# Kernel optimization log

Measured on AMD Instinct MI355X. Metric: run time of the kernel, lower is better.

The kernel has to match this reference:

```python
import jax, jax.numpy as jnp
import numpy as np

N_NODES = 100000
N_EDGES = 3200000
N_GRAPHS = 64
IN_DIM = 8
HIDDEN = 128
N_CLASSES = 10


def _glorot(key, fan_in, fan_out):
    s = 1.0 / np.sqrt(fan_in)
    return jax.random.uniform(key, (fan_in, fan_out), jnp.float32, -s, s)


def setup_inputs() -> dict:
    key = jax.random.key(0)
    ks = jax.random.split(key, 16)
    x = jax.random.normal(ks[0], (N_NODES, IN_DIM), jnp.float32)
    edge_index = jax.random.randint(ks[1], (2, N_EDGES), 0, N_NODES, jnp.int64)
    batch = jnp.sort(jax.random.randint(ks[2], (N_NODES,), 0, N_GRAPHS, jnp.int64))
    inp = {"x": x, "edge_index": edge_index, "batch": batch}
    dims = [(IN_DIM, HIDDEN)] + [(HIDDEN, HIDDEN)] * 4
    for i, (fi, fo) in enumerate(dims, start=1):
        inp[f"W{i}"] = _glorot(ks[2 + i], fi, fo)
        inp[f"b{i}"] = jnp.zeros((fo,), jnp.float32)
    inp["Wout"] = _glorot(ks[10], HIDDEN, N_CLASSES)
    inp["bout"] = jnp.zeros((N_CLASSES,), jnp.float32)
    return inp


def reference(x, edge_index, batch, W1, b1, W2, b2, W3, b3, W4, b4, W5, b5, Wout, bout):
    src, dst = edge_index[0], edge_index[1]
    E = src.shape[0]
    # GCN symmetric normalization with self-loops: deg computed on dst (col)
    deg = jax.ops.segment_sum(jnp.ones((E,), x.dtype), dst, num_segments=N_NODES) + 1.0
    dis = jax.lax.rsqrt(deg)                      # deg^{-1/2}, [N]
    enorm = dis[src] * dis[dst]                   # per-edge coeff, [E]
    self_coef = 1.0 / deg                         # self-loop coeff, [N]

    def gcn_conv(h, W, b):
        h = h @ W                                 # [N, F_out]
        msg = h[src] * enorm[:, None]             # gather + scale, [E, F_out]
        agg = jax.ops.segment_sum(msg, dst, num_segments=N_NODES)
        agg = agg + self_coef[:, None] * h        # fused self-loop term
        return agg + b

    h = jax.nn.relu(gcn_conv(x, W1, b1))
    h = jax.nn.relu(gcn_conv(h, W2, b2))
    h = jax.nn.relu(gcn_conv(h, W3, b3))
    h = jax.nn.relu(gcn_conv(h, W4, b4))
    h = jax.nn.relu(gcn_conv(h, W5, b5))

    # global mean pool per graph
    counts = jax.ops.segment_sum(jnp.ones((N_NODES,), h.dtype), batch, num_segments=N_GRAPHS)
    sums = jax.ops.segment_sum(h, batch, num_segments=N_GRAPHS)
    pooled = sums / jnp.maximum(counts, 1.0)[:, None]   # [G, HIDDEN]

    logits = pooled @ Wout + bout
    return jax.nn.log_softmax(logits, axis=1)
```

## Files before the change

kernel.cpp:

```cpp
#include <hip/hip_runtime.h>
#include <hip/hip_fp16.h>

#define N_NODES 100000
#define N_EDGES 3200000
#define N_GRAPHS 64
#define HID 128
#define NBUCK 782
#define NPART 256
#define EPB (N_EDGES / NPART)

typedef _Float16 half8 __attribute__((ext_vector_type(8)));
typedef float floatx4 __attribute__((ext_vector_type(4)));
typedef float floatx2 __attribute__((ext_vector_type(2)));

__device__ inline unsigned char f32_to_fp8(float v) {
    int p = __builtin_amdgcn_cvt_pk_fp8_f32(v, v, 0, false);
    return (unsigned char)(p & 0xff);
}

__global__ __launch_bounds__(256) void hist_kernel(const int* __restrict__ dst,
                                                   int* __restrict__ hist_g) {
    __shared__ int lh[NBUCK];
    int t = threadIdx.x, b = blockIdx.x;
    for (int j = t; j < NBUCK; j += 256) lh[j] = 0;
    __syncthreads();
    int beg = b * EPB, end = beg + EPB;
    for (int i = beg + t; i < end; i += 256) atomicAdd(&lh[dst[i] >> 7], 1);
    __syncthreads();
    for (int j = t; j < NBUCK; j += 256) hist_g[j * NPART + b] = lh[j];
}

__global__ __launch_bounds__(1024) void scan_hist(int* __restrict__ hist_g,
                                                  int* __restrict__ bb,
                                                  int* __restrict__ row_ptrN) {
    __shared__ int tot[1024];
    int t = threadIdx.x;
    int sum = 0;
    if (t < NBUCK) {
        const int4* h4 = (const int4*)(hist_g + t * NPART);
        for (int b = 0; b < NPART / 4; b++) {
            int4 v = h4[b];
            sum += v.x + v.y + v.z + v.w;
        }
    }
    tot[t] = sum;
    __syncthreads();
    for (int off = 1; off < 1024; off <<= 1) {
        int x = (t >= off) ? tot[t - off] : 0;
        __syncthreads();
        tot[t] += x;
        __syncthreads();
    }
    int excl = tot[t] - sum;
    if (t < NBUCK) {
        bb[t] = excl;
        int run = excl;
        int4* h4 = (int4*)(hist_g + t * NPART);
        for (int b = 0; b < NPART / 4; b++) {
            int4 v = h4[b];
            int4 o;
            o.x = run; run += v.x;
            o.y = run; run += v.y;
            o.z = run; run += v.z;
            o.w = run; run += v.w;
            h4[b] = o;
        }
    }
    if (t == NBUCK - 1) {
        bb[NBUCK] = excl + sum;
        row_ptrN[0] = excl + sum;
    }
}

__global__ __launch_bounds__(256) void part_kernel(const int* __restrict__ src,
                                                   const int* __restrict__ dst,
                                                   const int* __restrict__ hist_g,
                                                   int2* __restrict__ ebuf) {
    __shared__ int lf[NBUCK];
    int t = threadIdx.x, b = blockIdx.x;
    for (int j = t; j < NBUCK; j += 256) lf[j] = hist_g[j * NPART + b];
    __syncthreads();
    int beg = b * EPB, end = beg + EPB;
    for (int i = beg + t; i < end; i += 256) {
        int s = src[i], d = dst[i];
        int pos = atomicAdd(&lf[d >> 7], 1);
        ebuf[pos] = make_int2(s, d);
    }
}

__global__ __launch_bounds__(256) void build_kernel(const int2* __restrict__ ebuf,
                                                    const int* __restrict__ bb,
                                                    int* __restrict__ row_ptr,
                                                    int* __restrict__ col,
                                                    float* __restrict__ dis, int n) {
    __shared__ int c[128], fl[128], sc[128];
    int t = threadIdx.x, k = blockIdx.x;
    if (t < 128) c[t] = 0;
    __syncthreads();
    int beg = bb[k], end = bb[k + 1];
    for (int i = beg + t; i < end; i += 256) atomicAdd(&c[ebuf[i].y & 127], 1);
    __syncthreads();
    if (t < 128) sc[t] = c[t];
    __syncthreads();
    for (int off = 1; off < 128; off <<= 1) {
        int x = (t >= off && t < 128) ? sc[t - off] : 0;
        __syncthreads();
        if (t < 128) sc[t] += x;
        __syncthreads();
    }
    if (t < 128) {
        int rb = beg + sc[t] - c[t];
        fl[t] = rb;
        int node = k * 128 + t;
        if (node < n) {
            row_ptr[node] = rb;
            dis[node] = rsqrtf((float)c[t] + 1.0f);
        }
    }
    __syncthreads();
    for (int i = beg + t; i < end; i += 256) {
        int2 e = ebuf[i];
        int pos = atomicAdd(&fl[e.y & 127], 1);
        col[pos] = e.x;
    }
}

__global__ void prep_kernel(const float* __restrict__ x, const float* __restrict__ dis,
                            __half* __restrict__ g1, int n) {
    int i = blockIdx.x * blockDim.x + threadIdx.x;
    if (i < n) {
        float ds = dis[i];
        const float4* xr = (const float4*)(x + (size_t)i * 8);
        float4 x0 = xr[0], x1 = xr[1];
        __half2 h0 = __floats2half2_rn(ds * x0.x, ds * x0.y);
        __half2 h1 = __floats2half2_rn(ds * x0.z, ds * x0.w);
        __half2 h2 = __floats2half2_rn(ds * x1.x, ds * x1.y);
        __half2 h3 = __floats2half2_rn(ds * x1.z, ds * x1.w);
        uint2 v0, v1;
        v0.x = *(unsigned*)&h0; v0.y = *(unsigned*)&h1;
        v1.x = *(unsigned*)&h2; v1.y = *(unsigned*)&h3;
        uint2* o = (uint2*)(g1 + (size_t)i * 8);
        o[0] = v0; o[1] = v1;
    }
}

__global__ __launch_bounds__(256) void agg1_kernel(const __half* __restrict__ g1,
                                                   const int* __restrict__ row_ptr,
                                                   const int* __restrict__ col,
                                                   const float* __restrict__ dis,
                                                   float* __restrict__ p, int n) {
    int node = blockIdx.x * 4 + (threadIdx.x >> 6);
    if (node >= n) return;
    int lane = threadIdx.x & 63;
    int grp = lane >> 2;
    int fid = lane & 3;
    int beg = row_ptr[node], end = row_ptr[node + 1];
    float a0 = 0.f, a1 = 0.f;
    for (int e0 = beg; e0 < end; e0 += 16) {
        int m = end - e0;
        if (grp < m) {
            int c = col[e0 + grp];
            __half2 h2 = *(const __half2*)(g1 + (size_t)c * 8 + fid * 2);
            float2 f = __half22float2(h2);
            a0 += f.x; a1 += f.y;
        }
    }
    a0 += __shfl_xor(a0, 4);  a1 += __shfl_xor(a1, 4);
    a0 += __shfl_xor(a0, 8);  a1 += __shfl_xor(a1, 8);
    a0 += __shfl_xor(a0, 16); a1 += __shfl_xor(a1, 16);
    a0 += __shfl_xor(a0, 32); a1 += __shfl_xor(a1, 32);
    if (lane < 4) {
        __half2 own = *(const __half2*)(g1 + (size_t)node * 8 + fid * 2);
        float2 fo = __half22float2(own);
        float d = dis[node];
        *(float2*)(p + (size_t)node * 8 + fid * 2) = make_float2(d * (a0 + fo.x), d * (a1 + fo.y));
    }
}

__device__ inline uint2 f4_to_h4(float4 v) {
    __half2 a = __floats2half2_rn(v.x, v.y);
    __half2 b = __floats2half2_rn(v.z, v.w);
    uint2 r;
    r.x = *(unsigned*)&a;
    r.y = *(unsigned*)&b;
    return r;
}

__global__ __launch_bounds__(256) void gemm_k8(const float* __restrict__ A,
                                               const float* __restrict__ W,
                                               const float* __restrict__ bias,
                                               __half* __restrict__ out, int n) {
    __shared__ float4 Ws[8 * 32];
    const float4* W4 = (const float4*)W;
    for (int i = threadIdx.x; i < 8 * 32; i += 256) Ws[i] = W4[i];
    __syncthreads();
    int r = blockIdx.x * 256 + threadIdx.x;
    if (r >= n) return;
    float4 acc[32];
    #pragma unroll
    for (int j = 0; j < 32; j++) acc[j] = make_float4(0.f, 0.f, 0.f, 0.f);
    const float4* Arow = (const float4*)(A + (size_t)r * 8);
    float4 a0 = Arow[0], a1 = Arow[1];
    float av[8] = {a0.x, a0.y, a0.z, a0.w, a1.x, a1.y, a1.z, a1.w};
    #pragma unroll
    for (int kk = 0; kk < 8; kk++) {
        float a = av[kk];
        #pragma unroll
        for (int j = 0; j < 32; j++) {
            float4 w = Ws[kk * 32 + j];
            acc[j].x += a * w.x;
            acc[j].y += a * w.y;
            acc[j].z += a * w.z;
            acc[j].w += a * w.w;
        }
    }
    uint2* o = (uint2*)(out + (size_t)r * HID);
    const float4* b4 = (const float4*)bias;
    #pragma unroll
    for (int j = 0; j < 32; j++) {
        float4 b = b4[j];
        float4 v = make_float4(fmaxf(acc[j].x + b.x, 0.f), fmaxf(acc[j].y + b.y, 0.f),
                               fmaxf(acc[j].z + b.z, 0.f), fmaxf(acc[j].w + b.w, 0.f));
        o[j] = f4_to_h4(v);
    }
}

__global__ __launch_bounds__(128) void wconv(const float* __restrict__ W,
                                             __half* __restrict__ Wt) {
    int j = blockIdx.x, k = threadIdx.x;
    Wt[j * 128 + k] = __float2half(W[k * 128 + j]);
}

__global__ __launch_bounds__(256) void gemm_mfma(const __half* __restrict__ A,
                                                 const __half* __restrict__ Wt,
                                                 const float* __restrict__ dis,
                                                 unsigned char* __restrict__ outq, int n) {
    __shared__ uint4 wt_lds[128 * 17];
    __shared__ uint4 a_lds[64 * 17];
    int t = threadIdx.x;
    const uint4* Wg = (const uint4*)Wt;
    #pragma unroll
    for (int i = 0; i < 8; i++) {
        int idx = i * 256 + t;
        int j = idx >> 4, kq = idx & 15;
        wt_lds[j * 17 + kq] = Wg[idx];
    }
    int base = blockIdx.x * 64;
    const uint4* Ag = (const uint4*)A;
    #pragma unroll
    for (int i = 0; i < 4; i++) {
        int idx = i * 256 + t;
        int r = idx >> 4, kq = idx & 15;
        int row = base + r;
        if (row >= n) row = n - 1;
        a_lds[r * 17 + kq] = Ag[(size_t)row * 16 + kq];
    }
    __syncthreads();
    int w = t >> 6, lane = t & 63;
    int m = lane & 15, quad = lane >> 4;
    floatx4 acc[8];
    #pragma unroll
    for (int jt = 0; jt < 8; jt++) acc[jt] = (floatx4)(0.f);
    #pragma unroll
    for (int kc = 0; kc < 4; kc++) {
        uint4 araw = a_lds[(w * 16 + m) * 17 + kc * 4 + quad];
        half8 af = *(half8*)&araw;
        #pragma unroll
        for (int jt = 0; jt < 8; jt++) {
            uint4 braw = wt_lds[(jt * 16 + m) * 17 + kc * 4 + quad];
            half8 bf = *(half8*)&braw;
            acc[jt] = __builtin_amdgcn_mfma_f32_16x16x32_f16(af, bf, acc[jt], 0, 0, 0);
        }
    }
    #pragma unroll
    for (int reg = 0; reg < 4; reg++) {
        int row = base + w * 16 + quad * 4 + reg;
        if (row < n) {
            float ds = dis[row];
            #pragma unroll
            for (int jt = 0; jt < 8; jt++) {
                outq[(size_t)row * 128 + jt * 16 + m] = f32_to_fp8(acc[jt][reg] * ds);
            }
        }
    }
}

__global__ __launch_bounds__(256) void agg_kernel(const unsigned char* __restrict__ gq,
                                                  const int* __restrict__ row_ptr,
                                                  const int* __restrict__ col,
                                                  const float* __restrict__ dis,
                                                  const float* __restrict__ bias,
                                                  __half* __restrict__ out, int n) {
    int node = blockIdx.x * 4 + (threadIdx.x >> 6);
    if (node >= n) return;
    int lane = threadIdx.x & 63;
    int grp = lane >> 4;
    int fl = (lane & 15) * 8;
    int beg = row_ptr[node], end = row_ptr[node + 1];
    floatx2 a01 = {0.f, 0.f}, a23 = {0.f, 0.f}, a45 = {0.f, 0.f}, a67 = {0.f, 0.f};
    for (int e0 = beg; e0 < end; e0 += 64) {
        int m = min(64, end - e0);
        int cl = (lane < m) ? col[e0 + lane] : 0;
        int full = m >> 4;
        for (int j = 0; j < full; j++) {
            int c[4];
            #pragma unroll
            for (int u = 0; u < 4; u++) c[u] = __shfl(cl, j * 16 + u * 4 + grp);
            uint2 raw[4];
            #pragma unroll
            for (int u = 0; u < 4; u++)
                raw[u] = *(const uint2*)(gq + (size_t)c[u] * 128 + fl);
            #pragma unroll
            for (int u = 0; u < 4; u++) {
                a01 += __builtin_amdgcn_cvt_pk_f32_fp8(raw[u].x, false);
                a23 += __builtin_amdgcn_cvt_pk_f32_fp8(raw[u].x, true);
                a45 += __builtin_amdgcn_cvt_pk_f32_fp8(raw[u].y, false);
                a67 += __builtin_amdgcn_cvt_pk_f32_fp8(raw[u].y, true);
            }
        }
        for (int j4 = full * 16; j4 < m; j4 += 4) {
            int idx = j4 + grp;
            int c = __shfl(cl, idx & 63);
            float val = (idx < m) ? 1.f : 0.f;
            uint2 raw = *(const uint2*)(gq + (size_t)c * 128 + fl);
            floatx2 f0 = __builtin_amdgcn_cvt_pk_f32_fp8(raw.x, false);
            floatx2 f1 = __builtin_amdgcn_cvt_pk_f32_fp8(raw.x, true);
            floatx2 f2 = __builtin_amdgcn_cvt_pk_f32_fp8(raw.y, false);
            floatx2 f3 = __builtin_amdgcn_cvt_pk_f32_fp8(raw.y, true);
            a01 += val * f0;
            a23 += val * f1;
            a45 += val * f2;
            a67 += val * f3;
        }
    }
    float a[8] = {a01[0], a01[1], a23[0], a23[1], a45[0], a45[1], a67[0], a67[1]};
    #pragma unroll
    for (int k = 0; k < 8; k++) {
        a[k] += __shfl_xor(a[k], 16);
        a[k] += __shfl_xor(a[k], 32);
    }
    if (lane < 16) {
        float d = dis[node];
        uint2 own = *(const uint2*)(gq + (size_t)node * 128 + fl);
        floatx2 s0 = __builtin_amdgcn_cvt_pk_f32_fp8(own.x, false);
        floatx2 s1 = __builtin_amdgcn_cvt_pk_f32_fp8(own.x, true);
        floatx2 s2 = __builtin_amdgcn_cvt_pk_f32_fp8(own.y, false);
        floatx2 s3 = __builtin_amdgcn_cvt_pk_f32_fp8(own.y, true);
        float sv[8] = {s0[0], s0[1], s1[0], s1[1], s2[0], s2[1], s3[0], s3[1]};
        float4 b0 = *(const float4*)(bias + fl);
        float4 b1 = *(const float4*)(bias + fl + 4);
        float bv[8] = {b0.x, b0.y, b0.z, b0.w, b1.x, b1.y, b1.z, b1.w};
        float o[8];
        #pragma unroll
        for (int k = 0; k < 8; k++) o[k] = fmaxf(d * (a[k] + sv[k]) + bv[k], 0.f);
        uint4 q;
        __half2 q0 = __floats2half2_rn(o[0], o[1]);
        __half2 q1 = __floats2half2_rn(o[2], o[3]);
        __half2 q2 = __floats2half2_rn(o[4], o[5]);
        __half2 q3 = __floats2half2_rn(o[6], o[7]);
        q.x = *(unsigned*)&q0;
        q.y = *(unsigned*)&q1;
        q.z = *(unsigned*)&q2;
        q.w = *(unsigned*)&q3;
        *(uint4*)(out + (size_t)node * HID + fl) = q;
    }
}

__global__ __launch_bounds__(128) void gbounds_kernel(const int* __restrict__ batch,
                                                      int* __restrict__ bnd,
                                                      int* __restrict__ gcnt) {
    int g = threadIdx.x;
    if (g <= N_GRAPHS) {
        int lo = 0, hi = N_NODES;
        while (lo < hi) {
            int mid = (lo + hi) >> 1;
            if (batch[mid] < g) lo = mid + 1;
            else hi = mid;
        }
        bnd[g] = lo;
    }
    __syncthreads();
    if (g < N_GRAPHS) gcnt[g] = bnd[g + 1] - bnd[g];
}

__global__ __launch_bounds__(128) void pool_kernel(const __half* __restrict__ h,
                                                   const int* __restrict__ batch,
                                                   float* __restrict__ pooled, int n) {
    int f = threadIdx.x;
    int n0 = blockIdx.x * 64;
    if (n0 >= n) return;
    int n1 = min(n0 + 64, n);
    float acc = 0.f;
    int cur = batch[n0];
    for (int i = n0; i < n1; i++) {
        int b = batch[i];
        if (b != cur) {
            atomicAdd(&pooled[cur * HID + f], acc);
            acc = 0.f;
            cur = b;
        }
        acc += __half2float(h[(size_t)i * HID + f]);
    }
    atomicAdd(&pooled[cur * HID + f], acc);
}

__global__ __launch_bounds__(128) void final_kernel(const float* __restrict__ pooled,
                                                    const int* __restrict__ gcnt,
                                                    const float* __restrict__ Wout,
                                                    const float* __restrict__ bout,
                                                    float* __restrict__ out) {
    __shared__ float p[HID];
    __shared__ float lg[10];
    __shared__ float lsum;
    int g = blockIdx.x, t = threadIdx.x;
    float c = fmaxf((float)gcnt[g], 1.0f);
    p[t] = pooled[g * HID + t] / c;
    __syncthreads();
    if (t < 10) {
        float s = bout[t];
        for (int f = 0; f < HID; f++) s += p[f] * Wout[f * 10 + t];
        lg[t] = s;
    }
    __syncthreads();
    if (t == 0) {
        float m = lg[0];
        for (int ci = 1; ci < 10; ci++) m = fmaxf(m, lg[ci]);
        float se = 0.f;
        for (int ci = 0; ci < 10; ci++) se += expf(lg[ci] - m);
        lsum = m + logf(se);
    }
    __syncthreads();
    if (t < 10) out[g * 10 + t] = lg[t] - lsum;
}

extern "C" void kernel_launch(void* const* d_in, const int* in_sizes, int n_in,
                              void* d_out, int out_size, void* d_ws, size_t ws_size,
                              hipStream_t stream) {
    const float* x = (const float*)d_in[0];
    const int* ei = (const int*)d_in[1];
    const int* batch = (const int*)d_in[2];
    const float* W[5] = {(const float*)d_in[3], (const float*)d_in[5], (const float*)d_in[7],
                         (const float*)d_in[9], (const float*)d_in[11]};
    const float* B[5] = {(const float*)d_in[4], (const float*)d_in[6], (const float*)d_in[8],
                         (const float*)d_in[10], (const float*)d_in[12]};
    const float* Wout = (const float*)d_in[13];
    const float* bout = (const float*)d_in[14];
    float* out = (float*)d_out;

    const int* src = ei;
    const int* dst = ei + N_EDGES;

    char* ws = (char*)d_ws;
    size_t off = 0;
    auto alloc = [&](size_t bytes) -> char* {
        char* p = ws + off;
        off = (off + bytes + 255) & ~(size_t)255;
        return p;
    };
    float* pooled = (float*)alloc(N_GRAPHS * HID * 4);
    size_t zero_span = off;
    int* gcnt = (int*)alloc(N_GRAPHS * 4);
    int* bnd = (int*)alloc((N_GRAPHS + 1) * 4);
    int* row_ptr = (int*)alloc((N_NODES + 1) * 4);
    float* dis = (float*)alloc(N_NODES * 4);
    int* hist_g = (int*)alloc((size_t)NBUCK * NPART * 4);
    int* bb = (int*)alloc((NBUCK + 1) * 4);
    int2* ebuf = (int2*)alloc((size_t)N_EDGES * 8);
    int* col = (int*)alloc((size_t)N_EDGES * 4);
    __half* wt = (__half*)alloc(4 * 128 * 128 * 2);
    __half* g1 = (__half*)alloc((size_t)N_NODES * 8 * 2);
    float* p1 = (float*)alloc((size_t)N_NODES * 8 * 4);
    __half* h_a = (__half*)alloc((size_t)N_NODES * HID * 2);
    unsigned char* gq = (unsigned char*)alloc((size_t)N_NODES * HID);

    hipMemsetAsync(d_ws, 0, zero_span, stream);

    int nb = (N_NODES + 255) / 256;

    hist_kernel<<<NPART, 256, 0, stream>>>(dst, hist_g);
    scan_hist<<<1, 1024, 0, stream>>>(hist_g, bb, row_ptr + N_NODES);
    part_kernel<<<NPART, 256, 0, stream>>>(src, dst, hist_g, ebuf);
    build_kernel<<<NBUCK, 256, 0, stream>>>(ebuf, bb, row_ptr, col, dis, N_NODES);

    prep_kernel<<<nb, 256, 0, stream>>>(x, dis, g1, N_NODES);
    gbounds_kernel<<<1, 128, 0, stream>>>(batch, bnd, gcnt);
    for (int l = 1; l < 5; l++)
        wconv<<<128, 128, 0, stream>>>(W[l], wt + (size_t)(l - 1) * 128 * 128);

    int gb = (N_NODES + 255) / 256;
    int ab = (N_NODES + 3) / 4;
    int mb = (N_NODES + 63) / 64;

    agg1_kernel<<<ab, 256, 0, stream>>>(g1, row_ptr, col, dis, p1, N_NODES);
    gemm_k8<<<gb, 256, 0, stream>>>(p1, W[0], B[0], h_a, N_NODES);
    for (int l = 1; l < 5; l++) {
        gemm_mfma<<<mb, 256, 0, stream>>>(h_a, wt + (size_t)(l - 1) * 128 * 128, dis, gq,
                                          N_NODES);
        agg_kernel<<<ab, 256, 0, stream>>>(gq, row_ptr, col, dis, B[l], h_a, N_NODES);
    }

    pool_kernel<<<(N_NODES + 63) / 64, 128, 0, stream>>>(h_a, batch, pooled, N_NODES);
    final_kernel<<<N_GRAPHS, 128, 0, stream>>>(pooled, gcnt, Wout, bout, out);
}
```

Before: 625.8 us.

## Split single-block histogram scan into parallel wave-level reduce, scan, offset kernels

Replaces the one-block scan_hist kernel, where each thread serially summed and rewrote 256 per-partition counts, with three kernels. The first is a wave-per-bucket reduction of totals, the second a small single-block scan over the bucket totals, and the third a wave-per-bucket scan that writes the per-partition offsets. This is meant to remove a serial bottleneck in the edge-sorting preprocessing, at the cost of two extra kernel launches and a small temporary buffer.

```diff
diff --git a/kernel.cpp b/kernel.cpp
--- a/kernel.cpp
+++ b/kernel.cpp
@@ -30,46 +30,62 @@
     for (int j = t; j < NBUCK; j += 256) hist_g[j * NPART + b] = lh[j];
 }
 
-__global__ __launch_bounds__(1024) void scan_hist(int* __restrict__ hist_g,
-                                                  int* __restrict__ bb,
-                                                  int* __restrict__ row_ptrN) {
-    __shared__ int tot[1024];
+__global__ __launch_bounds__(256) void tot_kernel(const int* __restrict__ hist_g,
+                                                  int* __restrict__ tot) {
+    int wave = blockIdx.x * 4 + (threadIdx.x >> 6);
+    if (wave >= NBUCK) return;
+    int lane = threadIdx.x & 63;
+    const int4* h4 = (const int4*)(hist_g + (size_t)wave * NPART);
+    int4 v = h4[lane];
+    int s = v.x + v.y + v.z + v.w;
+    #pragma unroll
+    for (int off = 32; off > 0; off >>= 1) s += __shfl_down(s, off, 64);
+    if (lane == 0) tot[wave] = s;
+}
+
+__global__ __launch_bounds__(1024) void scan_tot(const int* __restrict__ tot,
+                                                 int* __restrict__ bb,
+                                                 int* __restrict__ row_ptrN) {
+    __shared__ int buf[1024];
     int t = threadIdx.x;
-    int sum = 0;
-    if (t < NBUCK) {
-        const int4* h4 = (const int4*)(hist_g + t * NPART);
-        for (int b = 0; b < NPART / 4; b++) {
-            int4 v = h4[b];
-            sum += v.x + v.y + v.z + v.w;
-        }
-    }
-    tot[t] = sum;
+    int v = (t < NBUCK) ? tot[t] : 0;
+    buf[t] = v;
     __syncthreads();
     for (int off = 1; off < 1024; off <<= 1) {
-        int x = (t >= off) ? tot[t - off] : 0;
+        int x = (t >= off) ? buf[t - off] : 0;
         __syncthreads();
-        tot[t] += x;
+        buf[t] += x;
         __syncthreads();
     }
-    int excl = tot[t] - sum;
-    if (t < NBUCK) {
-        bb[t] = excl;
-        int run = excl;
-        int4* h4 = (int4*)(hist_g + t * NPART);
-        for (int b = 0; b < NPART / 4; b++) {
-            int4 v = h4[b];
-            int4 o;
-            o.x = run; run += v.x;
-            o.y = run; run += v.y;
-            o.z = run; run += v.z;
-            o.w = run; run += v.w;
-            h4[b] = o;
-        }
-    }
+    if (t < NBUCK) bb[t] = buf[t] - v;
     if (t == NBUCK - 1) {
-        bb[NBUCK] = excl + sum;
-        row_ptrN[0] = excl + sum;
-    }
+        bb[NBUCK] = buf[t];
+        row_ptrN[0] = buf[t];
+    }
+}
+
+__global__ __launch_bounds__(256) void offs_kernel(int* __restrict__ hist_g,
+                                                   const int* __restrict__ bb) {
+    int wave = blockIdx.x * 4 + (threadIdx.x >> 6);
+    if (wave >= NBUCK) return;
+    int lane = threadIdx.x & 63;
+    int4* h4 = (int4*)(hist_g + (size_t)wave * NPART);
+    int4 v = h4[lane];
+    int s = v.x + v.y + v.z + v.w;
+    int e = s;
+    #pragma unroll
+    for (int off = 1; off < 64; off <<= 1) {
+        int x = __shfl_up(e, off, 64);
+        if (lane >= off) e += x;
+    }
+    e -= s;
+    int base = bb[wave] + e;
+    int4 o;
+    o.x = base; base += v.x;
+    o.y = base; base += v.y;
+    o.z = base; base += v.z;
+    o.w = base;
+    h4[lane] = o;
 }
 
 __global__ __launch_bounds__(256) void part_kernel(const int* __restrict__ src,
@@ -464,6 +480,7 @@
     int* row_ptr = (int*)alloc((N_NODES + 1) * 4);
     float* dis = (float*)alloc(N_NODES * 4);
     int* hist_g = (int*)alloc((size_t)NBUCK * NPART * 4);
+    int* tot = (int*)alloc(NBUCK * 4);
     int* bb = (int*)alloc((NBUCK + 1) * 4);
     int2* ebuf = (int2*)alloc((size_t)N_EDGES * 8);
     int* col = (int*)alloc((size_t)N_EDGES * 4);
@@ -476,9 +493,12 @@
     hipMemsetAsync(d_ws, 0, zero_span, stream);
 
     int nb = (N_NODES + 255) / 256;
+    int wb = (NBUCK + 3) / 4;
 
     hist_kernel<<<NPART, 256, 0, stream>>>(dst, hist_g);
-    scan_hist<<<1, 1024, 0, stream>>>(hist_g, bb, row_ptr + N_NODES);
+    tot_kernel<<<wb, 256, 0, stream>>>(hist_g, tot);
+    scan_tot<<<1, 1024, 0, stream>>>(tot, bb, row_ptr + N_NODES);
+    offs_kernel<<<wb, 256, 0, stream>>>(hist_g, bb);
     part_kernel<<<NPART, 256, 0, stream>>>(src, dst, hist_g, ebuf);
     build_kernel<<<NBUCK, 256, 0, stream>>>(ebuf, bb, row_ptr, col, dis, N_NODES);
 
```

Measured after the change: 558.4 us. 1.12x faster.
